# Performance work log

Hardware: AMD Instinct MI355X
Metric: run time of the kernel (lower is better)

Reference implementation:

```python
import jax, jax.numpy as jnp
import numpy as np

N = 50000      # nodes
E = 800000     # edges
D_IN = 128     # raw feature dim
H = 96         # hidden_channels
K = 8          # experts
L = 4          # num_layers
C = 40         # classes


def setup_inputs() -> dict:
    key = jax.random.key(0)
    ks = jax.random.split(key, 10)
    stdv = 1.0 / np.sqrt(H)
    inp = {
        'x': jax.random.normal(ks[0], (N, D_IN), dtype=jnp.float32),
        'edge_index': jax.random.randint(ks[1], (2, E), 0, N, dtype=jnp.int64),
        # fcs[0]: Linear(d, hidden); fcs[1]: Linear(hidden, c)
        'fc0_w': jax.random.normal(ks[2], (D_IN, H), dtype=jnp.float32) * 0.05,
        'fc0_b': jnp.zeros((H,), dtype=jnp.float32),
        'fc1_w': jax.random.normal(ks[3], (H, C), dtype=jnp.float32) * 0.05,
        'fc1_b': jnp.zeros((C,), dtype=jnp.float32),
        # context_enc (method='node'): per-layer Linear(hidden, K)
        'ctx_w': jax.random.normal(ks[4], (L, H, K), dtype=jnp.float32) * 0.05,
        'ctx_b': jnp.zeros((L, K), dtype=jnp.float32),
        # GraphMultiConvolution weights: [L, K, hidden, hidden], uniform(-stdv, stdv)
        'conv_w': jax.random.uniform(ks[5], (L, K, H, H), dtype=jnp.float32,
                                     minval=-stdv, maxval=stdv),
    }
    return inp


def reference(x, edge_index, fc0_w, fc0_b, fc1_w, fc1_b, ctx_w, ctx_b, conv_w):
    # eval-mode forward (training=False): no dropout, softmax routing
    row = edge_index[0]
    col = edge_index[1]
    h = jax.nn.relu(x @ fc0_w + fc0_b)                     # [N, H]
    for i in range(L):
        # routing logits and soft expert weights z: [N, K]
        z = jax.nn.softmax(h @ ctx_w[i] + ctx_b[i], axis=-1)
        # spmm aggregation: hi[r] = sum over edges (r, c) of h[c]
        hi = jax.ops.segment_sum(h[col], row, num_segments=N)  # [N, H]
        # K-expert batched matmul: [N, K, H]
        outs = jnp.einsum('nd,kdo->nko', hi, conv_w[i])
        # gumbel/softmax-weighted combine + residual
        out = jnp.einsum('nk,nko->no', z, outs) + h
        h = jax.nn.relu(out)
    return h @ fc1_w + fc1_b                               # [N, C]
```

## Files before the change

kernel.cpp:

```cpp
#include <hip/hip_runtime.h>

#define N_NODES 50000
#define N_EDGES 800000
#define DIN     128
#define H       96
#define K_EXP   8
#define L_LAYERS 4
#define C_OUT   40

typedef _Float16 f16;
typedef f16 f16x2 __attribute__((ext_vector_type(2)));
typedef f16 f16x4 __attribute__((ext_vector_type(4)));
typedef f16 f16x8 __attribute__((ext_vector_type(8)));
typedef float f32x4 __attribute__((ext_vector_type(4)));


#define CONV_TOT (L_LAYERS * K_EXP * H * H)
#define FC0_TOT  (DIN * H)
#define FC1_TOT  (48 * H)
#define CNT_BLOCKS ((N_EDGES + 255) / 256)
#define CVT_BLOCKS ((CONV_TOT + FC0_TOT + FC1_TOT + 255) / 256)

__global__ __launch_bounds__(256) void count_convert(const int* __restrict__ row,
                                                     int* __restrict__ deg,
                                                     int* __restrict__ p,
                                                     const float* __restrict__ conv_w,
                                                     const float* __restrict__ fc0_w,
                                                     const float* __restrict__ fc1_w,
                                                     f16* __restrict__ wfrag,
                                                     f16* __restrict__ fc0t,
                                                     f16* __restrict__ fc1t) {
    int tid = threadIdx.x;
    if ((int)blockIdx.x < CNT_BLOCKS) {
        int i = blockIdx.x * 256 + tid;
        if (i < N_EDGES) p[i] = atomicAdd(&deg[row[i]], 1);
    } else {
        int i = ((int)blockIdx.x - CNT_BLOCKS) * 256 + tid;
        if (i < CONV_TOT) {
            int o = i % H;
            int t = i / H;
            int d = t % H;
            int lk = t / H;
            int ct = o >> 4, lc = o & 15;
            int ks = d >> 5, quad = (d >> 3) & 3, j = d & 7;
            wfrag[(size_t)lk * 9216 + ct * 1536 + ks * 512 + (quad * 16 + lc) * 8 + j] =
                (f16)conv_w[i];
        } else if (i < CONV_TOT + FC0_TOT) {
            int j = i - CONV_TOT;
            int o = j % H, d = j / H;
            fc0t[o * DIN + d] = (f16)fc0_w[j];
        } else if (i < CONV_TOT + FC0_TOT + FC1_TOT) {
            int j = i - CONV_TOT - FC0_TOT;
            int o = j / H, d = j % H;
            fc1t[j] = (o < C_OUT) ? (f16)fc1_w[d * C_OUT + o] : (f16)0.f;
        }
    }
}

__global__ __launch_bounds__(1024) void scanA(const int* __restrict__ deg,
                                              int* __restrict__ rowptr,
                                              int* __restrict__ partial, int n) {
    __shared__ int wsum[16];
    int tid  = threadIdx.x;
    int lane = tid & 63, wid = tid >> 6;
    int idx = blockIdx.x * 1024 + tid;
    int v = (idx < n) ? deg[idx] : 0;
    int s = v;
    #pragma unroll
    for (int off = 1; off < 64; off <<= 1) {
        int t = __shfl_up(s, off, 64);
        if (lane >= off) s += t;
    }
    if (lane == 63) wsum[wid] = s;
    __syncthreads();
    if (wid == 0 && lane < 16) {
        int w = wsum[lane];
        #pragma unroll
        for (int off = 1; off < 16; off <<= 1) {
            int t = __shfl_up(w, off, 16);
            if (lane >= off) w += t;
        }
        wsum[lane] = w;
    }
    __syncthreads();
    int waveoff = (wid == 0) ? 0 : wsum[wid - 1];
    if (idx < n) rowptr[idx + 1] = waveoff + s;
    if (tid == 1023) partial[blockIdx.x] = waveoff + s;
}

__global__ __launch_bounds__(1024) void scanC(int* __restrict__ rowptr,
                                              const int* __restrict__ partial,
                                              int nb, int n) {
    __shared__ int boff_s;
    int tid = threadIdx.x;
    if (tid < 64) {
        int v = 0;
        for (int j = tid; j < (int)blockIdx.x; j += 64) v += partial[j];
        #pragma unroll
        for (int off = 32; off >= 1; off >>= 1) v += __shfl_xor(v, off, 64);
        if (tid == 0) boff_s = v;
    }
    __syncthreads();
    int boff = boff_s;
    int idx = blockIdx.x * 1024 + tid;
    if (idx == 0) rowptr[0] = 0;
    if (idx < n) rowptr[idx + 1] += boff;
}


#define SCT_BLOCKS 1024
#define FPAD 136

__global__ __launch_bounds__(256) void scatter_fc0(const int* __restrict__ row,
                                                   const int* __restrict__ col,
                                                   const int* __restrict__ p,
                                                   const int* __restrict__ rowptr,
                                                   int* __restrict__ csr,
                                                   const float* __restrict__ x,
                                                   const f16* __restrict__ fc0t,
                                                   const float* __restrict__ b,
                                                   f16* __restrict__ h16, int n) {
    __shared__ f16 As[64 * FPAD];
    __shared__ f16 Ws[96 * FPAD];
    int tid = threadIdx.x;
    if ((int)blockIdx.x < SCT_BLOCKS) {
        int stride = SCT_BLOCKS * 256;
        for (int i = blockIdx.x * 256 + tid; i < N_EDGES; i += stride)
            csr[rowptr[row[i]] + p[i]] = col[i];
        return;
    }
    int l = tid & 63, w = tid >> 6;
    int quad = l >> 4, lc = l & 15;
    int row0 = ((int)blockIdx.x - SCT_BLOCKS) * 64;

    for (int t = tid; t < 2048; t += 256) {
        int m = t >> 5, c4 = (t & 31) * 4;
        int gr = row0 + m;
        float4 v = {0.f, 0.f, 0.f, 0.f};
        if (gr < n) v = *(const float4*)(x + (size_t)gr * DIN + c4);
        f16x4 h4 = {(f16)v.x, (f16)v.y, (f16)v.z, (f16)v.w};
        *(f16x4*)&As[m * FPAD + c4] = h4;
    }
    for (int t = tid; t < 1536; t += 256) {
        int o = t >> 4, c8 = (t & 15) * 8;
        *(f16x8*)&Ws[o * FPAD + c8] = *(const f16x8*)(fc0t + o * DIN + c8);
    }
    __syncthreads();

    f16x8 afr[4];
    #pragma unroll
    for (int ks = 0; ks < 4; ks++)
        afr[ks] = *(const f16x8*)&As[(16 * w + lc) * FPAD + ks * 32 + quad * 8];

    f32x4 acc[6] = {};
    #pragma unroll
    for (int ct = 0; ct < 6; ct++) {
        #pragma unroll
        for (int ks = 0; ks < 4; ks++) {
            f16x8 bfr = *(const f16x8*)&Ws[(ct * 16 + lc) * FPAD + ks * 32 + quad * 8];
            acc[ct] = __builtin_amdgcn_mfma_f32_16x16x32_f16(afr[ks], bfr, acc[ct], 0, 0, 0);
        }
    }

    int m0 = 16 * w + quad * 4;
    #pragma unroll
    for (int r = 0; r < 4; r++) {
        int gr = row0 + m0 + r;
        if (gr < n) {
            #pragma unroll
            for (int ct = 0; ct < 6; ct++) {
                int o = ct * 16 + lc;
                h16[(size_t)gr * H + o] = (f16)fmaxf(acc[ct][r] + b[o], 0.f);
            }
        }
    }
}


#define LF_ROWS   64
#define LF_BLOCKS ((N_NODES + LF_ROWS - 1) / LF_ROWS)
#define HPAD      104

#define ACC8(v) { _Pragma("unroll") for (int q = 0; q < 8; q++) acc[q] += (float)(v)[q]; }

__global__ __launch_bounds__(256, 4) void layer_fused(const f16* __restrict__ h16,
                                                      const int* __restrict__ rowptr,
                                                      const int* __restrict__ csr,
                                                      const float* __restrict__ cw,
                                                      const float* __restrict__ cb,
                                                      const f16* __restrict__ wfrag,
                                                      f16* __restrict__ hout16, int n) {
    __shared__ f16 hi_lds[LF_ROWS * HPAD];
    __shared__ f16 Wl[9216];
    __shared__ f16 wsh[H * K_EXP];
    __shared__ float bs[K_EXP];

    int tid = threadIdx.x;
    int brow = blockIdx.x * LF_ROWS;

    for (int t = tid; t < H * K_EXP; t += 256) wsh[t] = (f16)cw[t];
    if (tid < K_EXP) bs[tid] = cb[tid];

    int l = tid & 63, w = tid >> 6;
    int quad = l >> 4, li = l & 15;

    {
        int g = tid >> 4, gl = tid & 15;
        bool act = gl < 12;
        const f16* hb = h16 + gl * 8;
        for (int sub = 0; sub < 4; sub++) {
            int r = brow + g * 4 + sub;
            float acc[8] = {};
            if (r < n) {
                int j = rowptr[r], e = rowptr[r + 1];
                int4 qa = *(const int4*)(csr + j);
                int4 qb = *(const int4*)(csr + j + 4);
                while (j + 8 <= e) {
                    int4 na = *(const int4*)(csr + j + 8);
                    int4 nb = *(const int4*)(csr + j + 12);
                    f16x8 v0 = {}, v1 = {}, v2 = {}, v3 = {}, v4 = {}, v5 = {}, v6 = {}, v7 = {};
                    if (act) {
                        v0 = *(const f16x8*)(hb + (size_t)qa.x * H);
                        v1 = *(const f16x8*)(hb + (size_t)qa.y * H);
                        v2 = *(const f16x8*)(hb + (size_t)qa.z * H);
                        v3 = *(const f16x8*)(hb + (size_t)qa.w * H);
                        v4 = *(const f16x8*)(hb + (size_t)qb.x * H);
                        v5 = *(const f16x8*)(hb + (size_t)qb.y * H);
                        v6 = *(const f16x8*)(hb + (size_t)qb.z * H);
                        v7 = *(const f16x8*)(hb + (size_t)qb.w * H);
                    }
                    ACC8(v0) ACC8(v1) ACC8(v2) ACC8(v3)
                    ACC8(v4) ACC8(v5) ACC8(v6) ACC8(v7)
                    j += 8; qa = na; qb = nb;
                }
                if (j + 4 <= e) {
                    f16x8 v0 = {}, v1 = {}, v2 = {}, v3 = {};
                    if (act) {
                        v0 = *(const f16x8*)(hb + (size_t)qa.x * H);
                        v1 = *(const f16x8*)(hb + (size_t)qa.y * H);
                        v2 = *(const f16x8*)(hb + (size_t)qa.z * H);
                        v3 = *(const f16x8*)(hb + (size_t)qa.w * H);
                    }
                    ACC8(v0) ACC8(v1) ACC8(v2) ACC8(v3)
                    j += 4; qa = qb;
                }
                int rem = e - j;
                if (rem > 0) {
                    f16x8 v0 = {}, v1 = {}, v2 = {};
                    if (act) {
                        v0 = *(const f16x8*)(hb + (size_t)qa.x * H);
                        if (rem > 1) v1 = *(const f16x8*)(hb + (size_t)qa.y * H);
                        if (rem > 2) v2 = *(const f16x8*)(hb + (size_t)qa.z * H);
                    }
                    ACC8(v0)
                    if (rem > 1) ACC8(v1)
                    if (rem > 2) ACC8(v2)
                }
            }
            if (act) {
                f16x8 o;
                #pragma unroll
                for (int q = 0; q < 8; q++) o[q] = (f16)acc[q];
                *(f16x8*)&hi_lds[(g * 4 + sub) * HPAD + gl * 8] = o;
            }
        }
    }
    __syncthreads();

    f16 zh[K_EXP];
    {
        float ca[K_EXP];
        #pragma unroll
        for (int k = 0; k < K_EXP; k++) ca[k] = 0.f;
        int node = brow + w * 16 + li;
        if (node < n) {
            const f16* hr = h16 + (size_t)node * H + quad * 24;
            #pragma unroll
            for (int c8 = 0; c8 < 3; c8++) {
                f16x8 v = *(const f16x8*)(hr + c8 * 8);
                #pragma unroll
                for (int jj = 0; jj < 8; jj++) {
                    float hv = (float)v[jj];
                    int d = quad * 24 + c8 * 8 + jj;
                    #pragma unroll
                    for (int k = 0; k < K_EXP; k++) ca[k] += hv * (float)wsh[d * K_EXP + k];
                }
            }
        }
        #pragma unroll
        for (int k = 0; k < K_EXP; k++) {
            ca[k] += __shfl_xor(ca[k], 16, 64);
            ca[k] += __shfl_xor(ca[k], 32, 64);
            ca[k] += bs[k];
        }
        float mx = ca[0];
        #pragma unroll
        for (int k = 1; k < K_EXP; k++) mx = fmaxf(mx, ca[k]);
        float ssum = 0.f;
        #pragma unroll
        for (int k = 0; k < K_EXP; k++) { ca[k] = __expf(ca[k] - mx); ssum += ca[k]; }
        float inv = 1.f / ssum;
        #pragma unroll
        for (int k = 0; k < K_EXP; k++) zh[k] = (f16)(ca[k] * inv);
    }

    f16x8 afr[3];
    #pragma unroll
    for (int ks = 0; ks < 3; ks++)
        afr[ks] = *(const f16x8*)&hi_lds[(w * 16 + li) * HPAD + ks * 32 + quad * 8];

    f32x4 acc[6] = {};
    #pragma unroll
    for (int k = 0; k < K_EXP; k++) {
        if (k) __syncthreads();
        const f16* src = wfrag + (size_t)k * 9216;
        for (int t = tid; t < 1152; t += 256)
            *(f16x8*)&Wl[t * 8] = *(const f16x8*)(src + t * 8);
        __syncthreads();

        f16 s = zh[k];
        f16x8 as0 = afr[0] * s, as1 = afr[1] * s, as2 = afr[2] * s;
        #pragma unroll
        for (int ct = 0; ct < 6; ct++) {
            f16x8 b0 = *(const f16x8*)&Wl[ct * 1536 + 0 * 512 + l * 8];
            f16x8 b1 = *(const f16x8*)&Wl[ct * 1536 + 1 * 512 + l * 8];
            f16x8 b2 = *(const f16x8*)&Wl[ct * 1536 + 2 * 512 + l * 8];
            acc[ct] = __builtin_amdgcn_mfma_f32_16x16x32_f16(as0, b0, acc[ct], 0, 0, 0);
            acc[ct] = __builtin_amdgcn_mfma_f32_16x16x32_f16(as1, b1, acc[ct], 0, 0, 0);
            acc[ct] = __builtin_amdgcn_mfma_f32_16x16x32_f16(as2, b2, acc[ct], 0, 0, 0);
        }
    }

    #pragma unroll
    for (int r = 0; r < 4; r++) {
        int gr = brow + w * 16 + quad * 4 + r;
        if (gr < n) {
            #pragma unroll
            for (int ct = 0; ct < 6; ct++) {
                int o = ct * 16 + li;
                float v = fmaxf(acc[ct][r] + (float)h16[(size_t)gr * H + o], 0.f);
                hout16[(size_t)gr * H + o] = (f16)v;
            }
        }
    }
}


#define APAD 104

__global__ __launch_bounds__(256) void fc1_kernel(const f16* __restrict__ h16,
                                                  const f16* __restrict__ fc1t,
                                                  const float* __restrict__ b,
                                                  float* __restrict__ out, int n) {
    __shared__ f16 As[64 * APAD];
    __shared__ f16 Ws[48 * APAD];
    int tid = threadIdx.x;
    int l = tid & 63, w = tid >> 6;
    int quad = l >> 4, lc = l & 15;
    int row0 = blockIdx.x * 64;

    for (int t = tid; t < 768; t += 256) {
        int m = t / 12, c8 = (t % 12) * 8;
        int gr = row0 + m;
        f16x8 v = {};
        if (gr < n) v = *(const f16x8*)(h16 + (size_t)gr * H + c8);
        *(f16x8*)&As[m * APAD + c8] = v;
    }
    for (int t = tid; t < 576; t += 256) {
        int o = t / 12, c8 = (t % 12) * 8;
        *(f16x8*)&Ws[o * APAD + c8] = *(const f16x8*)(fc1t + o * H + c8);
    }
    __syncthreads();

    f16x8 afr[3];
    #pragma unroll
    for (int ks = 0; ks < 3; ks++)
        afr[ks] = *(const f16x8*)&As[(16 * w + lc) * APAD + ks * 32 + quad * 8];

    f32x4 acc[3] = {};
    #pragma unroll
    for (int ct = 0; ct < 3; ct++) {
        #pragma unroll
        for (int ks = 0; ks < 3; ks++) {
            f16x8 bfr = *(const f16x8*)&Ws[(ct * 16 + lc) * APAD + ks * 32 + quad * 8];
            acc[ct] = __builtin_amdgcn_mfma_f32_16x16x32_f16(afr[ks], bfr, acc[ct], 0, 0, 0);
        }
    }

    int m0 = 16 * w + quad * 4;
    #pragma unroll
    for (int r = 0; r < 4; r++) {
        int gr = row0 + m0 + r;
        if (gr < n) {
            #pragma unroll
            for (int ct = 0; ct < 3; ct++) {
                int o = ct * 16 + lc;
                if (o < C_OUT)
                    out[(size_t)gr * C_OUT + o] = acc[ct][r] + b[o];
            }
        }
    }
}


extern "C" void kernel_launch(void* const* d_in, const int* in_sizes, int n_in,
                              void* d_out, int out_size, void* d_ws, size_t ws_size,
                              hipStream_t stream) {
    const float* x      = (const float*)d_in[0];
    const int*   ei     = (const int*)d_in[1];
    const float* fc0_w  = (const float*)d_in[2];
    const float* fc0_b  = (const float*)d_in[3];
    const float* fc1_w  = (const float*)d_in[4];
    const float* fc1_b  = (const float*)d_in[5];
    const float* ctx_w  = (const float*)d_in[6];
    const float* ctx_b  = (const float*)d_in[7];
    const float* conv_w = (const float*)d_in[8];
    float* out = (float*)d_out;

    const size_t NH = (size_t)N_NODES * H;

    f16*   h16a = (f16*)d_ws;
    f16*   h16b = h16a + NH;
    f16*   wfrag= h16b + NH;
    f16*   fc0t = wfrag + CONV_TOT;
    f16*   fc1t = fc0t + FC0_TOT;
    int* rowptr = (int*)(fc1t + FC1_TOT);
    int* deg    = rowptr + (N_NODES + 1);
    int* csr    = deg + N_NODES;
    int* prank  = csr + N_EDGES;
    int* partial  = prank + N_EDGES;

    const int* row = ei;
    const int* col = ei + N_EDGES;

    hipMemsetAsync(deg, 0, sizeof(int) * N_NODES, stream);

    count_convert<<<CNT_BLOCKS + CVT_BLOCKS, 256, 0, stream>>>(
        row, deg, prank, conv_w, fc0_w, fc1_w, wfrag, fc0t, fc1t);
    int nsb = (N_NODES + 1023) / 1024;
    scanA<<<nsb, 1024, 0, stream>>>(deg, rowptr, partial, N_NODES);
    scanC<<<nsb, 1024, 0, stream>>>(rowptr, partial, nsb, N_NODES);

    int gemm_grid = (N_NODES + 63) / 64;
    scatter_fc0<<<SCT_BLOCKS + gemm_grid, 256, 0, stream>>>(
        row, col, prank, rowptr, csr, x, fc0t, fc0_b, h16a, N_NODES);

    f16* hcur = h16a;
    f16* hnext = h16b;
    for (int i = 0; i < L_LAYERS; i++) {
        layer_fused<<<LF_BLOCKS, 256, 0, stream>>>(
            hcur, rowptr, csr,
            ctx_w + (size_t)i * H * K_EXP, ctx_b + (size_t)i * K_EXP,
            wfrag + (size_t)i * K_EXP * H * H, hnext, N_NODES);
        f16* t = hcur; hcur = hnext; hnext = t;
    }
    fc1_kernel<<<gemm_grid, 256, 0, stream>>>(hcur, fc1t, fc1_b, out, N_NODES);
}
```

Baseline: 326.4 us.

## Fuse fc1 into last layer kernel and stage expert weights in pairs

The final output projection (fc1) now runs inside the last layer_fused launch, using the relu'd tile kept in LDS. This removes a separate kernel and one global round-trip of the hidden state. Expert weights are now staged two experts at a time in a doubled LDS buffer, and the first pair is prefetched before aggregation, which halves the number of block-wide barriers. The larger LDS footprint may reduce the number of resident blocks per CU.

New measurement: 396.6 us. 1.22x slower.

```diff
diff --git a/kernel.cpp b/kernel.cpp
--- a/kernel.cpp
+++ b/kernel.cpp
@@ -189,17 +189,25 @@
                                                       const float* __restrict__ cw,
                                                       const float* __restrict__ cb,
                                                       const f16* __restrict__ wfrag,
-                                                      f16* __restrict__ hout16, int n) {
+                                                      f16* __restrict__ hout16,
+                                                      const f16* __restrict__ fc1t_,
+                                                      const float* __restrict__ fc1b,
+                                                      float* __restrict__ out, int n) {
     __shared__ f16 hi_lds[LF_ROWS * HPAD];
-    __shared__ f16 Wl[9216];
+    __shared__ f16 Wl[2 * 9216];
     __shared__ f16 wsh[H * K_EXP];
     __shared__ float bs[K_EXP];
+    __shared__ float fb[48];
 
     int tid = threadIdx.x;
     int brow = blockIdx.x * LF_ROWS;
 
     for (int t = tid; t < H * K_EXP; t += 256) wsh[t] = (f16)cw[t];
     if (tid < K_EXP) bs[tid] = cb[tid];
+    if (fc1t_ && tid < 48) fb[tid] = (tid < C_OUT) ? fc1b[tid] : 0.f;
+
+    for (int t = tid; t < 2304; t += 256)
+        *(f16x8*)&Wl[t * 8] = *(const f16x8*)(wfrag + t * 8);
 
     int l = tid & 63, w = tid >> 6;
     int quad = l >> 4, li = l & 15;
@@ -311,92 +319,88 @@
 
     f32x4 acc[6] = {};
     #pragma unroll
-    for (int k = 0; k < K_EXP; k++) {
-        if (k) __syncthreads();
-        const f16* src = wfrag + (size_t)k * 9216;
-        for (int t = tid; t < 1152; t += 256)
-            *(f16x8*)&Wl[t * 8] = *(const f16x8*)(src + t * 8);
-        __syncthreads();
-
-        f16 s = zh[k];
-        f16x8 as0 = afr[0] * s, as1 = afr[1] * s, as2 = afr[2] * s;
-        #pragma unroll
-        for (int ct = 0; ct < 6; ct++) {
-            f16x8 b0 = *(const f16x8*)&Wl[ct * 1536 + 0 * 512 + l * 8];
-            f16x8 b1 = *(const f16x8*)&Wl[ct * 1536 + 1 * 512 + l * 8];
-            f16x8 b2 = *(const f16x8*)&Wl[ct * 1536 + 2 * 512 + l * 8];
-            acc[ct] = __builtin_amdgcn_mfma_f32_16x16x32_f16(as0, b0, acc[ct], 0, 0, 0);
-            acc[ct] = __builtin_amdgcn_mfma_f32_16x16x32_f16(as1, b1, acc[ct], 0, 0, 0);
-            acc[ct] = __builtin_amdgcn_mfma_f32_16x16x32_f16(as2, b2, acc[ct], 0, 0, 0);
-        }
-    }
-
-    #pragma unroll
-    for (int r = 0; r < 4; r++) {
-        int gr = brow + w * 16 + quad * 4 + r;
-        if (gr < n) {
+    for (int kb = 0; kb < K_EXP; kb += 2) {
+        if (kb) {
+            __syncthreads();
+            const f16* src = wfrag + (size_t)kb * 9216;
+            for (int t = tid; t < 2304; t += 256)
+                *(f16x8*)&Wl[t * 8] = *(const f16x8*)(src + t * 8);
+            __syncthreads();
+        }
+        #pragma unroll
+        for (int k2 = 0; k2 < 2; k2++) {
+            f16 s = zh[kb + k2];
+            f16x8 as0 = afr[0] * s, as1 = afr[1] * s, as2 = afr[2] * s;
+            const f16* wl = &Wl[k2 * 9216];
+            #pragma unroll
+            for (int ct = 0; ct < 6; ct++) {
+                f16x8 b0 = *(const f16x8*)&wl[ct * 1536 + 0 * 512 + l * 8];
+                f16x8 b1 = *(const f16x8*)&wl[ct * 1536 + 1 * 512 + l * 8];
+                f16x8 b2 = *(const f16x8*)&wl[ct * 1536 + 2 * 512 + l * 8];
+                acc[ct] = __builtin_amdgcn_mfma_f32_16x16x32_f16(as0, b0, acc[ct], 0, 0, 0);
+                acc[ct] = __builtin_amdgcn_mfma_f32_16x16x32_f16(as1, b1, acc[ct], 0, 0, 0);
+                acc[ct] = __builtin_amdgcn_mfma_f32_16x16x32_f16(as2, b2, acc[ct], 0, 0, 0);
+            }
+        }
+    }
+
+    if (fc1t_) {
+        #pragma unroll
+        for (int r = 0; r < 4; r++) {
+            int lr = w * 16 + quad * 4 + r;
+            int gr = brow + lr;
             #pragma unroll
             for (int ct = 0; ct < 6; ct++) {
                 int o = ct * 16 + li;
-                float v = fmaxf(acc[ct][r] + (float)h16[(size_t)gr * H + o], 0.f);
-                hout16[(size_t)gr * H + o] = (f16)v;
-            }
-        }
-    }
-}
-
-
-#define APAD 104
-
-__global__ __launch_bounds__(256) void fc1_kernel(const f16* __restrict__ h16,
-                                                  const f16* __restrict__ fc1t,
-                                                  const float* __restrict__ b,
-                                                  float* __restrict__ out, int n) {
-    __shared__ f16 As[64 * APAD];
-    __shared__ f16 Ws[48 * APAD];
-    int tid = threadIdx.x;
-    int l = tid & 63, w = tid >> 6;
-    int quad = l >> 4, lc = l & 15;
-    int row0 = blockIdx.x * 64;
-
-    for (int t = tid; t < 768; t += 256) {
-        int m = t / 12, c8 = (t % 12) * 8;
-        int gr = row0 + m;
-        f16x8 v = {};
-        if (gr < n) v = *(const f16x8*)(h16 + (size_t)gr * H + c8);
-        *(f16x8*)&As[m * APAD + c8] = v;
-    }
-    for (int t = tid; t < 576; t += 256) {
-        int o = t / 12, c8 = (t % 12) * 8;
-        *(f16x8*)&Ws[o * APAD + c8] = *(const f16x8*)(fc1t + o * H + c8);
-    }
-    __syncthreads();
-
-    f16x8 afr[3];
-    #pragma unroll
-    for (int ks = 0; ks < 3; ks++)
-        afr[ks] = *(const f16x8*)&As[(16 * w + lc) * APAD + ks * 32 + quad * 8];
-
-    f32x4 acc[3] = {};
-    #pragma unroll
-    for (int ct = 0; ct < 3; ct++) {
-        #pragma unroll
-        for (int ks = 0; ks < 3; ks++) {
-            f16x8 bfr = *(const f16x8*)&Ws[(ct * 16 + lc) * APAD + ks * 32 + quad * 8];
-            acc[ct] = __builtin_amdgcn_mfma_f32_16x16x32_f16(afr[ks], bfr, acc[ct], 0, 0, 0);
-        }
-    }
-
-    int m0 = 16 * w + quad * 4;
-    #pragma unroll
-    for (int r = 0; r < 4; r++) {
-        int gr = row0 + m0 + r;
-        if (gr < n) {
+                float v = 0.f;
+                if (gr < n) v = fmaxf(acc[ct][r] + (float)h16[(size_t)gr * H + o], 0.f);
+                hi_lds[lr * HPAD + o] = (f16)v;
+            }
+        }
+        __syncthreads();
+        for (int t = tid; t < 576; t += 256) {
+            int o = t / 12, c8 = (t % 12) * 8;
+            *(f16x8*)&Wl[o * HPAD + c8] = *(const f16x8*)(fc1t_ + o * H + c8);
+        }
+        __syncthreads();
+
+        f16x8 a2[3];
+        #pragma unroll
+        for (int ks = 0; ks < 3; ks++)
+            a2[ks] = *(const f16x8*)&hi_lds[(w * 16 + li) * HPAD + ks * 32 + quad * 8];
+
+        f32x4 acc3[3] = {};
+        #pragma unroll
+        for (int ct = 0; ct < 3; ct++) {
             #pragma unroll
-            for (int ct = 0; ct < 3; ct++) {
-                int o = ct * 16 + lc;
-                if (o < C_OUT)
-                    out[(size_t)gr * C_OUT + o] = acc[ct][r] + b[o];
+            for (int ks = 0; ks < 3; ks++) {
+                f16x8 bfr = *(const f16x8*)&Wl[(ct * 16 + li) * HPAD + ks * 32 + quad * 8];
+                acc3[ct] = __builtin_amdgcn_mfma_f32_16x16x32_f16(a2[ks], bfr, acc3[ct], 0, 0, 0);
+            }
+        }
+        #pragma unroll
+        for (int r = 0; r < 4; r++) {
+            int gr = brow + w * 16 + quad * 4 + r;
+            if (gr < n) {
+                #pragma unroll
+                for (int ct = 0; ct < 3; ct++) {
+                    int o = ct * 16 + li;
+                    if (o < C_OUT)
+                        out[(size_t)gr * C_OUT + o] = acc3[ct][r] + fb[o];
+                }
+            }
+        }
+    } else {
+        #pragma unroll
+        for (int r = 0; r < 4; r++) {
+            int gr = brow + w * 16 + quad * 4 + r;
+            if (gr < n) {
+                #pragma unroll
+                for (int ct = 0; ct < 6; ct++) {
+                    int o = ct * 16 + li;
+                    float v = fmaxf(acc[ct][r] + (float)h16[(size_t)gr * H + o], 0.f);
+                    hout16[(size_t)gr * H + o] = (f16)v;
+                }
             }
         }
     }
@@ -448,11 +452,12 @@
     f16* hcur = h16a;
     f16* hnext = h16b;
     for (int i = 0; i < L_LAYERS; i++) {
+        bool last = (i == L_LAYERS - 1);
         layer_fused<<<LF_BLOCKS, 256, 0, stream>>>(
             hcur, rowptr, csr,
             ctx_w + (size_t)i * H * K_EXP, ctx_b + (size_t)i * K_EXP,
-            wfrag + (size_t)i * K_EXP * H * H, hnext, N_NODES);
+            wfrag + (size_t)i * K_EXP * H * H, hnext,
+            last ? fc1t : (const f16*)nullptr, fc1_b, out, N_NODES);
         f16* t = hcur; hcur = hnext; hnext = t;
     }
-    fc1_kernel<<<gemm_grid, 256, 0, stream>>>(hcur, fc1t, fc1_b, out, N_NODES);
-}
+}
```
